# Kernel optimization log

Hardware: AMD Instinct MI355X
Metric: run time of the kernel (lower is better)

The kernel has to match this reference:

```python
import jax, jax.numpy as jnp
import numpy as np

B, L, D = 4, 2048, 1024
H, KD, VD = 16, 64, 64
EPS = 1e-5


def setup_inputs() -> dict:
    key = jax.random.key(0)
    ks = jax.random.split(key, 12)
    s_in = 1.0 / np.sqrt(D)
    s_out = 1.0 / np.sqrt(H * VD)
    return {
        "queries": jax.random.normal(ks[0], (B, L, D), dtype=jnp.float32),
        "Wq": jax.random.uniform(ks[1], (D, H * KD), jnp.float32, -s_in, s_in),
        "bq": jax.random.uniform(ks[2], (H * KD,), jnp.float32, -s_in, s_in),
        "Wk": jax.random.uniform(ks[3], (D, H * KD), jnp.float32, -s_in, s_in),
        "bk": jax.random.uniform(ks[4], (H * KD,), jnp.float32, -s_in, s_in),
        "Wv": jax.random.uniform(ks[5], (D, H * VD), jnp.float32, -s_in, s_in),
        "bv": jax.random.uniform(ks[6], (H * VD,), jnp.float32, -s_in, s_in),
        "Wo": jax.random.uniform(ks[7], (H * VD, D), jnp.float32, -s_out, s_out),
        "bo": jax.random.uniform(ks[8], (D,), jnp.float32, -s_out, s_out),
        "gamma": jnp.ones((D,), jnp.float32),
        "beta": jnp.zeros((D,), jnp.float32),
    }


def reference(queries, Wq, bq, Wk, bk, Wv, bv, Wo, bo, gamma, beta):
    # QKV projections -> [B, L, H, head_dim]
    q = (queries @ Wq + bq).reshape(B, L, H, KD)
    k = (queries @ Wk + bk).reshape(B, L, H, KD)
    v = (queries @ Wv + bv).reshape(B, L, H, VD)
    # scaled dot-product attention per head: scores [B, H, Lq, Lk]
    scores = jnp.einsum("bqhd,bkhd->bhqk", q, k) / np.sqrt(KD).astype(np.float32)
    attn = jax.nn.softmax(scores, axis=-1)
    out = jnp.einsum("bhqk,bkhd->bqhd", attn, v).reshape(B, L, H * VD)
    # out projection (dropout is identity in eval), residual + LayerNorm
    res = out @ Wo + bo + queries
    mu = jnp.mean(res, axis=-1, keepdims=True)
    var = jnp.var(res, axis=-1, keepdims=True)
    return (res - mu) / jnp.sqrt(var + EPS) * gamma + beta
```

## Files before the change

kernel.cpp:

```cpp
#include <hip/hip_runtime.h>
#include <hip/hip_bf16.h>

#define BATCH 4
#define SEQ   2048
#define DIM   1024
#define NHEAD 16
#define HDIM  64
#define EPS_LN 1e-5f
#define QSCALE 0.18033688011112042f

typedef __attribute__((ext_vector_type(8))) short short8;
typedef __attribute__((ext_vector_type(4))) float f32x4;

__device__ __forceinline__ unsigned short f2bf(float x) {
    __hip_bfloat16 h = __float2bfloat16(x);
    return *reinterpret_cast<unsigned short*>(&h);
}
__device__ __forceinline__ unsigned int pack2bf(float a, float b) {
    __hip_bfloat162 h = __float22bfloat162_rn(float2{a, b});
    return *reinterpret_cast<unsigned int*>(&h);
}

__device__ __forceinline__ void gl_lds16(const void* g, void* l) {
    __builtin_amdgcn_global_load_lds(
        (const __attribute__((address_space(1))) unsigned int*)g,
        (__attribute__((address_space(3))) unsigned int*)l,
        16, 0, 0);
}

__global__ __launch_bounds__(256) void convert_bf16(const float* __restrict__ in,
                                                    unsigned short* __restrict__ out)
{
    const int i = blockIdx.x * 256 + threadIdx.x;
    float4 v = ((const float4*)in)[i];
    ushort4 u;
    u.x = f2bf(v.x); u.y = f2bf(v.y); u.z = f2bf(v.z); u.w = f2bf(v.w);
    ((ushort4*)out)[i] = u;
}

__global__ __launch_bounds__(256) void transpose_convert(const float* __restrict__ W,
                                                         unsigned short* __restrict__ Wt,
                                                         int K, int N)
{
    __shared__ float Ts[64][65];
    const int k0 = blockIdx.y * 64, n0 = blockIdx.x * 64;
    const int t = threadIdx.x;
    const int lr = t >> 2, lq = t & 3;

#pragma unroll
    for (int i = 0; i < 4; i++) {
        float4 v = *(const float4*)(W + (size_t)(k0 + lr) * N + n0 + (lq * 4 + i) * 4);
        Ts[lr][(lq * 4 + i) * 4 + 0] = v.x;
        Ts[lr][(lq * 4 + i) * 4 + 1] = v.y;
        Ts[lr][(lq * 4 + i) * 4 + 2] = v.z;
        Ts[lr][(lq * 4 + i) * 4 + 3] = v.w;
    }
    __syncthreads();
#pragma unroll
    for (int i = 0; i < 4; i++) {
        const int c = lq * 16 + i * 4;
        ushort4 u;
        u.x = f2bf(Ts[c + 0][lr]);
        u.y = f2bf(Ts[c + 1][lr]);
        u.z = f2bf(Ts[c + 2][lr]);
        u.w = f2bf(Ts[c + 3][lr]);
        *(ushort4*)(Wt + (size_t)(n0 + lr) * K + k0 + c) = u;
    }
}

template <int MODE>
__global__ __launch_bounds__(256) void gemm_mfma(const unsigned short* __restrict__ A,
                                                 const unsigned short* __restrict__ Bt,
                                                 const float* __restrict__ bias,
                                                 const float* __restrict__ resid,
                                                 void* __restrict__ Cout,
                                                 int M, int N, int K, float scale)
{
    __shared__ __attribute__((aligned(16))) unsigned short As[128 * 32];
    __shared__ __attribute__((aligned(16))) unsigned short Bs[128 * 32];

    const int tid = threadIdx.x;
    const int w = tid >> 6, lane = tid & 63;
    const int col = lane & 15, quad = lane >> 4;
    const int wm = (w >> 1) * 64, wn = (w & 1) * 64;
    const int m0 = blockIdx.y * 128, n0 = blockIdx.x * 128;

    f32x4 acc[4][4] = {};

    const int srow = tid >> 2, sc4 = tid & 3;

    for (int k0 = 0; k0 < K; k0 += 32) {
        __syncthreads();
#pragma unroll
        for (int it = 0; it < 2; it++) {
            gl_lds16(A  + (size_t)(m0 + srow + it * 64) * K + k0 + sc4 * 8,
                     (char*)As + w * 1024 + it * 4096);
            gl_lds16(Bt + (size_t)(n0 + srow + it * 64) * K + k0 + sc4 * 8,
                     (char*)Bs + w * 1024 + it * 4096);
        }
        __syncthreads();

        short8 af[4], bf[4];
#pragma unroll
        for (int mt = 0; mt < 4; mt++) af[mt] = *(short8*)&As[(wm + mt * 16 + col) * 32 + quad * 8];
#pragma unroll
        for (int nt = 0; nt < 4; nt++) bf[nt] = *(short8*)&Bs[(wn + nt * 16 + col) * 32 + quad * 8];

#pragma unroll
        for (int mt = 0; mt < 4; mt++)
#pragma unroll
            for (int nt = 0; nt < 4; nt++)
                acc[mt][nt] = __builtin_amdgcn_mfma_f32_16x16x32_bf16(af[mt], bf[nt], acc[mt][nt], 0, 0, 0);
    }

#pragma unroll
    for (int nt = 0; nt < 4; nt++) {
        const int n = n0 + wn + nt * 16 + col;
        const float bv = bias[n];
#pragma unroll
        for (int mt = 0; mt < 4; mt++) {
            const int mbase = m0 + wm + mt * 16 + quad * 4;
            if (MODE == 0) {
#pragma unroll
                for (int r = 0; r < 4; r++)
                    ((unsigned short*)Cout)[(size_t)(mbase + r) * N + n] = f2bf((acc[mt][nt][r] + bv) * scale);
            } else if (MODE == 1) {
                const int h = n >> 6, d = n & 63;
                const int b = mbase >> 11, l = mbase & 2047;
                ushort4 u;
                u.x = f2bf(acc[mt][nt][0] + bv);
                u.y = f2bf(acc[mt][nt][1] + bv);
                u.z = f2bf(acc[mt][nt][2] + bv);
                u.w = f2bf(acc[mt][nt][3] + bv);
                *(ushort4*)((unsigned short*)Cout + ((size_t)((b * NHEAD + h) * HDIM + d)) * SEQ + l) = u;
            } else {
#pragma unroll
                for (int r = 0; r < 4; r++) {
                    const size_t off = (size_t)(mbase + r) * N + n;
                    ((float*)Cout)[off] = acc[mt][nt][r] + bv + resid[off];
                }
            }
        }
    }
}

#define KP 72
__global__ __launch_bounds__(256) void attn_mfma(const unsigned short* __restrict__ Qb,
                                                 const unsigned short* __restrict__ Kb,
                                                 const unsigned short* __restrict__ Vt,
                                                 unsigned short* __restrict__ Ob)
{
    __shared__ __attribute__((aligned(16))) unsigned short Ks[64 * KP];
    __shared__ __attribute__((aligned(16))) unsigned short Vs[64 * KP];
    __shared__ __attribute__((aligned(16))) unsigned short Ps[4][32 * KP];

    const int tid = threadIdx.x;
    const int w = tid >> 6, lane = tid & 63;
    const int col = lane & 15, quad = lane >> 4;

    const int nqt = SEQ / 128;
    const int qt_ = blockIdx.x % nqt;
    const int h   = (blockIdx.x / nqt) % NHEAD;
    const int b   = blockIdx.x / (nqt * NHEAD);

    const int q0 = qt_ * 128 + w * 32;

    short8 qf[2][2];
#pragma unroll
    for (int qt = 0; qt < 2; qt++) {
        const size_t base = ((size_t)(b * SEQ) + q0 + qt * 16 + col) * DIM + h * HDIM + quad * 8;
        qf[qt][0] = *(const short8*)(Qb + base);
        qf[qt][1] = *(const short8*)(Qb + base + 32);
    }

    short8 onesf;
    {
        const short one = (short)0x3F80;
        const short v = (col == 0) ? one : (short)0;
        onesf = short8{v, v, v, v, v, v, v, v};
    }

    f32x4 o[4][2] = {};
    f32x4 od[2]   = {};

    const size_t kbase0 = ((size_t)(b * SEQ)) * DIM + h * HDIM;
    const size_t vbase0 = ((size_t)((b * NHEAD + h) * HDIM)) * SEQ;

    const int srow = tid >> 3, sc = tid & 7;
    unsigned short* Pw = Ps[w];

    for (int kt = 0; kt < SEQ / 64; kt++) {
        __syncthreads();
#pragma unroll
        for (int it = 0; it < 2; it++) {
            const int row = srow + it * 32;
            *(int4*)&Ks[row * KP + sc * 8] = *(const int4*)(Kb + kbase0 + (size_t)(kt * 64 + row) * DIM + sc * 8);
            *(int4*)&Vs[row * KP + sc * 8] = *(const int4*)(Vt + vbase0 + (size_t)row * SEQ + kt * 64 + sc * 8);
        }
        __syncthreads();

#pragma unroll
        for (int nt = 0; nt < 4; nt++) {
            short8 kf0 = *(short8*)&Ks[(nt * 16 + col) * KP + quad * 8];
            short8 kf1 = *(short8*)&Ks[(nt * 16 + col) * KP + quad * 8 + 32];
#pragma unroll
            for (int qt = 0; qt < 2; qt++) {
                f32x4 s = {};
                s = __builtin_amdgcn_mfma_f32_16x16x32_bf16(kf0, qf[qt][0], s, 0, 0, 0);
                s = __builtin_amdgcn_mfma_f32_16x16x32_bf16(kf1, qf[qt][1], s, 0, 0, 0);
                const float p0 = __builtin_amdgcn_exp2f(s[0]);
                const float p1 = __builtin_amdgcn_exp2f(s[1]);
                const float p2 = __builtin_amdgcn_exp2f(s[2]);
                const float p3 = __builtin_amdgcn_exp2f(s[3]);
                uint2 pk;
                pk.x = pack2bf(p0, p1);
                pk.y = pack2bf(p2, p3);
                *(uint2*)&Pw[(qt * 16 + col) * KP + nt * 16 + quad * 4] = pk;
            }
        }

        short8 pf[2][2];
#pragma unroll
        for (int qt = 0; qt < 2; qt++) {
            pf[qt][0] = *(short8*)&Pw[(qt * 16 + col) * KP + quad * 8];
            pf[qt][1] = *(short8*)&Pw[(qt * 16 + col) * KP + quad * 8 + 32];
        }

#pragma unroll
        for (int qt = 0; qt < 2; qt++) {
            od[qt] = __builtin_amdgcn_mfma_f32_16x16x32_bf16(onesf, pf[qt][0], od[qt], 0, 0, 0);
            od[qt] = __builtin_amdgcn_mfma_f32_16x16x32_bf16(onesf, pf[qt][1], od[qt], 0, 0, 0);
        }

#pragma unroll
        for (int mt = 0; mt < 4; mt++) {
            short8 vf0 = *(short8*)&Vs[(mt * 16 + col) * KP + quad * 8];
            short8 vf1 = *(short8*)&Vs[(mt * 16 + col) * KP + quad * 8 + 32];
#pragma unroll
            for (int qt = 0; qt < 2; qt++) {
                o[mt][qt] = __builtin_amdgcn_mfma_f32_16x16x32_bf16(vf0, pf[qt][0], o[mt][qt], 0, 0, 0);
                o[mt][qt] = __builtin_amdgcn_mfma_f32_16x16x32_bf16(vf1, pf[qt][1], o[mt][qt], 0, 0, 0);
            }
        }
    }

#pragma unroll
    for (int qt = 0; qt < 2; qt++) {
        const float den = __shfl(od[qt][0], col);
        const float inv = 1.f / den;
        const size_t rowoff = ((size_t)(b * SEQ) + q0 + qt * 16 + col) * DIM + h * HDIM;
#pragma unroll
        for (int mt = 0; mt < 4; mt++) {
            ushort4 u;
            u.x = f2bf(o[mt][qt][0] * inv);
            u.y = f2bf(o[mt][qt][1] * inv);
            u.z = f2bf(o[mt][qt][2] * inv);
            u.w = f2bf(o[mt][qt][3] * inv);
            *(ushort4*)(Ob + rowoff + mt * 16 + quad * 4) = u;
        }
    }
}

__global__ __launch_bounds__(256) void layernorm_kernel(float* __restrict__ res,
                                                        const float* __restrict__ gamma,
                                                        const float* __restrict__ beta)
{
    const int tid = threadIdx.x;
    const int row = blockIdx.x;
    float4 xv = ((const float4*)(res + (size_t)row * DIM))[tid];

    float s  = xv.x + xv.y + xv.z + xv.w;
    float sq = xv.x * xv.x + xv.y * xv.y + xv.z * xv.z + xv.w * xv.w;
#pragma unroll
    for (int off = 32; off; off >>= 1) {
        s  += __shfl_xor(s, off);
        sq += __shfl_xor(sq, off);
    }
    __shared__ float sm[8];
    const int w = tid >> 6, lane = tid & 63;
    if (lane == 0) { sm[w] = s; sm[4 + w] = sq; }
    __syncthreads();
    const float st  = sm[0] + sm[1] + sm[2] + sm[3];
    const float sqt = sm[4] + sm[5] + sm[6] + sm[7];
    const float mu   = st * (1.f / DIM);
    const float var  = sqt * (1.f / DIM) - mu * mu;
    const float rstd = rsqrtf(var + EPS_LN);

    float4 g  = ((const float4*)gamma)[tid];
    float4 be = ((const float4*)beta)[tid];
    float4 o;
    o.x = (xv.x - mu) * rstd * g.x + be.x;
    o.y = (xv.y - mu) * rstd * g.y + be.y;
    o.z = (xv.z - mu) * rstd * g.z + be.z;
    o.w = (xv.w - mu) * rstd * g.w + be.w;
    ((float4*)(res + (size_t)row * DIM))[tid] = o;
}

extern "C" void kernel_launch(void* const* d_in, const int* in_sizes, int n_in,
                              void* d_out, int out_size, void* d_ws, size_t ws_size,
                              hipStream_t stream)
{
    const float* queries = (const float*)d_in[0];
    const float* Wq = (const float*)d_in[1];
    const float* bq = (const float*)d_in[2];
    const float* Wk = (const float*)d_in[3];
    const float* bk = (const float*)d_in[4];
    const float* Wv = (const float*)d_in[5];
    const float* bv = (const float*)d_in[6];
    const float* Wo = (const float*)d_in[7];
    const float* bo = (const float*)d_in[8];
    const float* gamma = (const float*)d_in[9];
    const float* beta  = (const float*)d_in[10];
    float* outp = (float*)d_out;

    const int M = BATCH * SEQ;
    const size_t BUF = (size_t)M * DIM;
    const size_t WSZ = (size_t)DIM * DIM;

    unsigned short* w0  = (unsigned short*)d_ws;
    unsigned short* qin = w0;
    unsigned short* Qbf = w0 + BUF;
    unsigned short* Kbf = w0 + 2 * BUF;
    unsigned short* Vtb = w0 + 3 * BUF;
    unsigned short* Wqt = w0 + 4 * BUF;
    unsigned short* Wkt = Wqt + WSZ;
    unsigned short* Wvt = Wqt + 2 * WSZ;
    unsigned short* Wot = Wqt + 3 * WSZ;
    unsigned short* Obf = qin;

    dim3 blk(256);

    convert_bf16<<<BUF / 4 / 256, blk, 0, stream>>>(queries, qin);

    dim3 tgrid(DIM / 64, DIM / 64);
    transpose_convert<<<tgrid, blk, 0, stream>>>(Wq, Wqt, DIM, DIM);
    transpose_convert<<<tgrid, blk, 0, stream>>>(Wk, Wkt, DIM, DIM);
    transpose_convert<<<tgrid, blk, 0, stream>>>(Wv, Wvt, DIM, DIM);
    transpose_convert<<<tgrid, blk, 0, stream>>>(Wo, Wot, DIM, DIM);

    dim3 ggrid(DIM / 128, M / 128);
    gemm_mfma<0><<<ggrid, blk, 0, stream>>>(qin, Wqt, bq, nullptr, Qbf, M, DIM, DIM, QSCALE);
    gemm_mfma<0><<<ggrid, blk, 0, stream>>>(qin, Wkt, bk, nullptr, Kbf, M, DIM, DIM, 1.0f);
    gemm_mfma<1><<<ggrid, blk, 0, stream>>>(qin, Wvt, bv, nullptr, Vtb, M, DIM, DIM, 1.0f);

    attn_mfma<<<BATCH * NHEAD * (SEQ / 128), blk, 0, stream>>>(Qbf, Kbf, Vtb, Obf);

    gemm_mfma<2><<<ggrid, blk, 0, stream>>>(Obf, Wot, bo, queries, outp, M, DIM, DIM, 1.0f);

    layernorm_kernel<<<M, blk, 0, stream>>>(outp, gamma, beta);
}
```

Before: 358.0 us.

## Fuse QKV projections into one GEMM launch and load V fragments directly

Merges the four weight transpose launches into a single 3D-grid launch. It also merges the Q, K and V projection GEMMs into one launch over a concatenated weight matrix, choosing bias and output layout per column sector. In attention, V tiles no longer go through shared memory; each wave loads its V fragments straight from global memory into registers. The aim is to cut launch overhead, give the GEMM a larger grid for better occupancy, and shrink LDS traffic in attention, at the cost of redundant global V reads across waves.

```diff
diff --git a/kernel.cpp b/kernel.cpp
--- a/kernel.cpp
+++ b/kernel.cpp
@@ -38,18 +38,25 @@
     ((ushort4*)out)[i] = u;
 }
 
-__global__ __launch_bounds__(256) void transpose_convert(const float* __restrict__ W,
-                                                         unsigned short* __restrict__ Wt,
-                                                         int K, int N)
+__global__ __launch_bounds__(256) void transpose_convert4(const float* __restrict__ W0,
+                                                          const float* __restrict__ W1,
+                                                          const float* __restrict__ W2,
+                                                          const float* __restrict__ W3,
+                                                          unsigned short* __restrict__ Wqkvt,
+                                                          unsigned short* __restrict__ Wot)
 {
     __shared__ float Ts[64][65];
+    const int z = blockIdx.z;
+    const float* W = (z == 0) ? W0 : (z == 1) ? W1 : (z == 2) ? W2 : W3;
+    unsigned short* Wt = (z == 3) ? Wot : (Wqkvt + (size_t)z * DIM * DIM);
+
     const int k0 = blockIdx.y * 64, n0 = blockIdx.x * 64;
     const int t = threadIdx.x;
     const int lr = t >> 2, lq = t & 3;
 
 #pragma unroll
     for (int i = 0; i < 4; i++) {
-        float4 v = *(const float4*)(W + (size_t)(k0 + lr) * N + n0 + (lq * 4 + i) * 4);
+        float4 v = *(const float4*)(W + (size_t)(k0 + lr) * DIM + n0 + (lq * 4 + i) * 4);
         Ts[lr][(lq * 4 + i) * 4 + 0] = v.x;
         Ts[lr][(lq * 4 + i) * 4 + 1] = v.y;
         Ts[lr][(lq * 4 + i) * 4 + 2] = v.z;
@@ -64,17 +71,18 @@
         u.y = f2bf(Ts[c + 1][lr]);
         u.z = f2bf(Ts[c + 2][lr]);
         u.w = f2bf(Ts[c + 3][lr]);
-        *(ushort4*)(Wt + (size_t)(n0 + lr) * K + k0 + c) = u;
-    }
-}
-
-template <int MODE>
-__global__ __launch_bounds__(256) void gemm_mfma(const unsigned short* __restrict__ A,
-                                                 const unsigned short* __restrict__ Bt,
-                                                 const float* __restrict__ bias,
-                                                 const float* __restrict__ resid,
-                                                 void* __restrict__ Cout,
-                                                 int M, int N, int K, float scale)
+        *(ushort4*)(Wt + (size_t)(n0 + lr) * DIM + k0 + c) = u;
+    }
+}
+
+__global__ __launch_bounds__(256) void gemm_qkv(const unsigned short* __restrict__ A,
+                                                const unsigned short* __restrict__ Bt,
+                                                const float* __restrict__ bq,
+                                                const float* __restrict__ bk,
+                                                const float* __restrict__ bv,
+                                                unsigned short* __restrict__ Qbf,
+                                                unsigned short* __restrict__ Kbf,
+                                                unsigned short* __restrict__ Vtb)
 {
     __shared__ __attribute__((aligned(16))) unsigned short As[128 * 32];
     __shared__ __attribute__((aligned(16))) unsigned short Bs[128 * 32];
@@ -86,16 +94,15 @@
     const int m0 = blockIdx.y * 128, n0 = blockIdx.x * 128;
 
     f32x4 acc[4][4] = {};
-
     const int srow = tid >> 2, sc4 = tid & 3;
 
-    for (int k0 = 0; k0 < K; k0 += 32) {
+    for (int k0 = 0; k0 < DIM; k0 += 32) {
         __syncthreads();
 #pragma unroll
         for (int it = 0; it < 2; it++) {
-            gl_lds16(A  + (size_t)(m0 + srow + it * 64) * K + k0 + sc4 * 8,
+            gl_lds16(A  + (size_t)(m0 + srow + it * 64) * DIM + k0 + sc4 * 8,
                      (char*)As + w * 1024 + it * 4096);
-            gl_lds16(Bt + (size_t)(n0 + srow + it * 64) * K + k0 + sc4 * 8,
+            gl_lds16(Bt + (size_t)(n0 + srow + it * 64) * DIM + k0 + sc4 * 8,
                      (char*)Bs + w * 1024 + it * 4096);
         }
         __syncthreads();
@@ -113,32 +120,92 @@
                 acc[mt][nt] = __builtin_amdgcn_mfma_f32_16x16x32_bf16(af[mt], bf[nt], acc[mt][nt], 0, 0, 0);
     }
 
+    const int sector = n0 >> 10;
+    const float* bias = (sector == 0) ? bq : (sector == 1) ? bk : bv;
+
 #pragma unroll
     for (int nt = 0; nt < 4; nt++) {
         const int n = n0 + wn + nt * 16 + col;
-        const float bv = bias[n];
+        const int nloc = n - (sector << 10);
+        const float bvv = bias[nloc];
 #pragma unroll
         for (int mt = 0; mt < 4; mt++) {
             const int mbase = m0 + wm + mt * 16 + quad * 4;
-            if (MODE == 0) {
+            if (sector == 0) {
 #pragma unroll
                 for (int r = 0; r < 4; r++)
-                    ((unsigned short*)Cout)[(size_t)(mbase + r) * N + n] = f2bf((acc[mt][nt][r] + bv) * scale);
-            } else if (MODE == 1) {
-                const int h = n >> 6, d = n & 63;
+                    Qbf[(size_t)(mbase + r) * DIM + nloc] = f2bf((acc[mt][nt][r] + bvv) * QSCALE);
+            } else if (sector == 1) {
+#pragma unroll
+                for (int r = 0; r < 4; r++)
+                    Kbf[(size_t)(mbase + r) * DIM + nloc] = f2bf(acc[mt][nt][r] + bvv);
+            } else {
+                const int h = nloc >> 6, d = nloc & 63;
                 const int b = mbase >> 11, l = mbase & 2047;
                 ushort4 u;
-                u.x = f2bf(acc[mt][nt][0] + bv);
-                u.y = f2bf(acc[mt][nt][1] + bv);
-                u.z = f2bf(acc[mt][nt][2] + bv);
-                u.w = f2bf(acc[mt][nt][3] + bv);
-                *(ushort4*)((unsigned short*)Cout + ((size_t)((b * NHEAD + h) * HDIM + d)) * SEQ + l) = u;
-            } else {
-#pragma unroll
-                for (int r = 0; r < 4; r++) {
-                    const size_t off = (size_t)(mbase + r) * N + n;
-                    ((float*)Cout)[off] = acc[mt][nt][r] + bv + resid[off];
-                }
+                u.x = f2bf(acc[mt][nt][0] + bvv);
+                u.y = f2bf(acc[mt][nt][1] + bvv);
+                u.z = f2bf(acc[mt][nt][2] + bvv);
+                u.w = f2bf(acc[mt][nt][3] + bvv);
+                *(ushort4*)(Vtb + ((size_t)((b * NHEAD + h) * HDIM + d)) * SEQ + l) = u;
+            }
+        }
+    }
+}
+
+__global__ __launch_bounds__(256) void gemm_out(const unsigned short* __restrict__ A,
+                                                const unsigned short* __restrict__ Bt,
+                                                const float* __restrict__ bias,
+                                                const float* __restrict__ resid,
+                                                float* __restrict__ Cout)
+{
+    __shared__ __attribute__((aligned(16))) unsigned short As[128 * 32];
+    __shared__ __attribute__((aligned(16))) unsigned short Bs[128 * 32];
+
+    const int tid = threadIdx.x;
+    const int w = tid >> 6, lane = tid & 63;
+    const int col = lane & 15, quad = lane >> 4;
+    const int wm = (w >> 1) * 64, wn = (w & 1) * 64;
+    const int m0 = blockIdx.y * 128, n0 = blockIdx.x * 128;
+
+    f32x4 acc[4][4] = {};
+    const int srow = tid >> 2, sc4 = tid & 3;
+
+    for (int k0 = 0; k0 < DIM; k0 += 32) {
+        __syncthreads();
+#pragma unroll
+        for (int it = 0; it < 2; it++) {
+            gl_lds16(A  + (size_t)(m0 + srow + it * 64) * DIM + k0 + sc4 * 8,
+                     (char*)As + w * 1024 + it * 4096);
+            gl_lds16(Bt + (size_t)(n0 + srow + it * 64) * DIM + k0 + sc4 * 8,
+                     (char*)Bs + w * 1024 + it * 4096);
+        }
+        __syncthreads();
+
+        short8 af[4], bf[4];
+#pragma unroll
+        for (int mt = 0; mt < 4; mt++) af[mt] = *(short8*)&As[(wm + mt * 16 + col) * 32 + quad * 8];
+#pragma unroll
+        for (int nt = 0; nt < 4; nt++) bf[nt] = *(short8*)&Bs[(wn + nt * 16 + col) * 32 + quad * 8];
+
+#pragma unroll
+        for (int mt = 0; mt < 4; mt++)
+#pragma unroll
+            for (int nt = 0; nt < 4; nt++)
+                acc[mt][nt] = __builtin_amdgcn_mfma_f32_16x16x32_bf16(af[mt], bf[nt], acc[mt][nt], 0, 0, 0);
+    }
+
+#pragma unroll
+    for (int nt = 0; nt < 4; nt++) {
+        const int n = n0 + wn + nt * 16 + col;
+        const float bvv = bias[n];
+#pragma unroll
+        for (int mt = 0; mt < 4; mt++) {
+            const int mbase = m0 + wm + mt * 16 + quad * 4;
+#pragma unroll
+            for (int r = 0; r < 4; r++) {
+                const size_t off = (size_t)(mbase + r) * DIM + n;
+                Cout[off] = acc[mt][nt][r] + bvv + resid[off];
             }
         }
     }
@@ -151,7 +218,6 @@
                                                  unsigned short* __restrict__ Ob)
 {
     __shared__ __attribute__((aligned(16))) unsigned short Ks[64 * KP];
-    __shared__ __attribute__((aligned(16))) unsigned short Vs[64 * KP];
     __shared__ __attribute__((aligned(16))) unsigned short Ps[4][32 * KP];
 
     const int tid = threadIdx.x;
@@ -175,8 +241,7 @@
 
     short8 onesf;
     {
-        const short one = (short)0x3F80;
-        const short v = (col == 0) ? one : (short)0;
+        const short v = (col == 0) ? (short)0x3F80 : (short)0;
         onesf = short8{v, v, v, v, v, v, v, v};
     }
 
@@ -195,9 +260,16 @@
         for (int it = 0; it < 2; it++) {
             const int row = srow + it * 32;
             *(int4*)&Ks[row * KP + sc * 8] = *(const int4*)(Kb + kbase0 + (size_t)(kt * 64 + row) * DIM + sc * 8);
-            *(int4*)&Vs[row * KP + sc * 8] = *(const int4*)(Vt + vbase0 + (size_t)row * SEQ + kt * 64 + sc * 8);
-        }
-        __syncthreads();
+        }
+        __syncthreads();
+
+        short8 vf[4][2];
+#pragma unroll
+        for (int mt = 0; mt < 4; mt++) {
+            const size_t va = vbase0 + (size_t)(mt * 16 + col) * SEQ + kt * 64 + quad * 8;
+            vf[mt][0] = *(const short8*)(Vt + va);
+            vf[mt][1] = *(const short8*)(Vt + va + 32);
+        }
 
 #pragma unroll
         for (int nt = 0; nt < 4; nt++) {
@@ -233,15 +305,12 @@
         }
 
 #pragma unroll
-        for (int mt = 0; mt < 4; mt++) {
-            short8 vf0 = *(short8*)&Vs[(mt * 16 + col) * KP + quad * 8];
-            short8 vf1 = *(short8*)&Vs[(mt * 16 + col) * KP + quad * 8 + 32];
+        for (int mt = 0; mt < 4; mt++)
 #pragma unroll
             for (int qt = 0; qt < 2; qt++) {
-                o[mt][qt] = __builtin_amdgcn_mfma_f32_16x16x32_bf16(vf0, pf[qt][0], o[mt][qt], 0, 0, 0);
-                o[mt][qt] = __builtin_amdgcn_mfma_f32_16x16x32_bf16(vf1, pf[qt][1], o[mt][qt], 0, 0, 0);
+                o[mt][qt] = __builtin_amdgcn_mfma_f32_16x16x32_bf16(vf[mt][0], pf[qt][0], o[mt][qt], 0, 0, 0);
+                o[mt][qt] = __builtin_amdgcn_mfma_f32_16x16x32_bf16(vf[mt][1], pf[qt][1], o[mt][qt], 0, 0, 0);
             }
-        }
     }
 
 #pragma unroll
@@ -322,30 +391,24 @@
     unsigned short* Qbf = w0 + BUF;
     unsigned short* Kbf = w0 + 2 * BUF;
     unsigned short* Vtb = w0 + 3 * BUF;
-    unsigned short* Wqt = w0 + 4 * BUF;
-    unsigned short* Wkt = Wqt + WSZ;
-    unsigned short* Wvt = Wqt + 2 * WSZ;
-    unsigned short* Wot = Wqt + 3 * WSZ;
+    unsigned short* Wqkvt = w0 + 4 * BUF;
+    unsigned short* Wot   = Wqkvt + 3 * WSZ;
     unsigned short* Obf = qin;
 
     dim3 blk(256);
 
     convert_bf16<<<BUF / 4 / 256, blk, 0, stream>>>(queries, qin);
 
-    dim3 tgrid(DIM / 64, DIM / 64);
-    transpose_convert<<<tgrid, blk, 0, stream>>>(Wq, Wqt, DIM, DIM);
-    transpose_convert<<<tgrid, blk, 0, stream>>>(Wk, Wkt, DIM, DIM);
-    transpose_convert<<<tgrid, blk, 0, stream>>>(Wv, Wvt, DIM, DIM);
-    transpose_convert<<<tgrid, blk, 0, stream>>>(Wo, Wot, DIM, DIM);
-
-    dim3 ggrid(DIM / 128, M / 128);
-    gemm_mfma<0><<<ggrid, blk, 0, stream>>>(qin, Wqt, bq, nullptr, Qbf, M, DIM, DIM, QSCALE);
-    gemm_mfma<0><<<ggrid, blk, 0, stream>>>(qin, Wkt, bk, nullptr, Kbf, M, DIM, DIM, 1.0f);
-    gemm_mfma<1><<<ggrid, blk, 0, stream>>>(qin, Wvt, bv, nullptr, Vtb, M, DIM, DIM, 1.0f);
+    dim3 tgrid(DIM / 64, DIM / 64, 4);
+    transpose_convert4<<<tgrid, blk, 0, stream>>>(Wq, Wk, Wv, Wo, Wqkvt, Wot);
+
+    dim3 qkvgrid(3 * DIM / 128, M / 128);
+    gemm_qkv<<<qkvgrid, blk, 0, stream>>>(qin, Wqkvt, bq, bk, bv, Qbf, Kbf, Vtb);
 
     attn_mfma<<<BATCH * NHEAD * (SEQ / 128), blk, 0, stream>>>(Qbf, Kbf, Vtb, Obf);
 
-    gemm_mfma<2><<<ggrid, blk, 0, stream>>>(Obf, Wot, bo, queries, outp, M, DIM, DIM, 1.0f);
+    dim3 ogrid(DIM / 128, M / 128);
+    gemm_out<<<ogrid, blk, 0, stream>>>(Obf, Wot, bo, queries, outp);
 
     layernorm_kernel<<<M, blk, 0, stream>>>(outp, gamma, beta);
 }
```

Result: slower. 417.2 us (+16.6%).
